# Kernel tuning notes

Hardware: AMD Instinct MI355X
Metric: run time of the kernel (lower is better)

The kernel has to match this reference:

```python
import jax, jax.numpy as jnp
import numpy as np

THRESH = 6.0   # latent_dist_threshold
SCALE = 1.0    # reward_scale
EPS = 1e-6


def _count_scatter(idx, vals):
    # idx, vals: [B, V, N]; counts[b,v,s] = sum of vals over queries whose argmin == s
    B, V, N = idx.shape
    bi = jnp.arange(B)[:, None, None]
    vi = jnp.arange(V)[None, :, None]
    return jnp.zeros((B, V, N), jnp.int32).at[bi, vi, idx].add(vals)


def _direction(min_dists, min_idx, query_xy, source_xy, query_mask):
    # one chamfer direction: queries matched to nearest source particles
    d = jnp.take_along_axis(source_xy, min_idx[..., None], axis=2)  # [B,V,N,2]
    dist = jnp.linalg.norm(query_xy - d, ord=2, axis=-1)            # [B,V,N]
    latent_mask = min_dists > THRESH
    rpm = query_mask | latent_mask                                   # reward_particle_mask
    vals = jnp.where(rpm, 0, 1).astype(jnp.int32)
    count = _count_scatter(min_idx, vals)                            # density counts per source
    w = 1.0 / (jnp.take_along_axis(count, min_idx, axis=2).astype(jnp.float32) + EPS)
    dist = jnp.where(rpm, 0.0, w * dist)
    unmatched = jnp.any((~query_mask) & latent_mask, axis=-1).astype(jnp.float32)
    groups = jnp.maximum(jnp.sum(count > 0, axis=2).astype(jnp.float32) + unmatched, 1.0)
    return -(jnp.sum(dist, axis=2) + unmatched) / groups             # [B,V]


def setup_inputs() -> dict:
    key = jax.random.key(0)
    k1, k2 = jax.random.split(key)
    achieved = jax.random.normal(k1, (256, 2, 512, 10), dtype=jnp.float32)
    desired = jax.random.normal(k2, (256, 2, 512, 10), dtype=jnp.float32)
    return {"achieved": achieved, "desired": desired}


def reference(achieved, desired):
    # latent_classifier=None -> obj_class_cond = ones -> mask = (ones == 0) = all False
    state_mask = jnp.zeros(achieved.shape[:-1], bool)
    goal_mask = jnp.zeros(desired.shape[:-1], bool)
    s_vis = achieved[..., 5:9]
    s_xy = achieved[..., :2]
    g_vis = desired[..., 5:9]
    g_xy = desired[..., :2]
    # 'l2_simple' pairwise squared dist: P[b,v,i,j] = ||s_vis_i - g_vis_j||^2
    P = (jnp.sum(s_vis ** 2, -1)[..., :, None]
         + jnp.sum(g_vis ** 2, -1)[..., None, :]
         - 2.0 * jnp.einsum('bvnd,bvmd->bvnm', s_vis, g_vis))
    P = jnp.where(state_mask[..., :, None] | goal_mask[..., None, :], jnp.inf, P)
    # goal -> state: min over state axis (2)
    md1 = jnp.min(P, axis=2)
    mi1 = jnp.argmin(P, axis=2).astype(jnp.int32)
    r_g2s = _direction(md1, mi1, g_xy, s_xy, goal_mask)
    # state -> goal: min over goal axis (3)
    md2 = jnp.min(P, axis=3)
    mi2 = jnp.argmin(P, axis=3).astype(jnp.int32)
    r_s2g = _direction(md2, mi2, s_xy, g_xy, state_mask)
    rv = (r_g2s + r_s2g) / 2.0                                       # [B,V]
    no_valid = jnp.all(goal_mask, -1) | jnp.all(state_mask, -1)
    rv = jnp.where(no_valid, -1.0, rv)
    reward = jnp.mean(rv, axis=1)
    return SCALE * reward[:, None]                                    # [B,1]
```

## Files before the change

kernel.cpp:

```cpp
#include <hip/hip_runtime.h>
#include <math.h>

#define NB 256
#define NV 2
#define NN 512
#define ND 10
#define THRESH_SQ 6.0f
#define EPS_W 1e-6f

typedef __attribute__((ext_vector_type(8))) short bf16x8;
typedef __attribute__((ext_vector_type(4))) float f32x4;

__device__ __forceinline__ unsigned short f2bf(float x) {
    union { float f; unsigned u; } v; v.f = x;
    unsigned r = v.u + 0x7FFFu + ((v.u >> 16) & 1u);
    return (unsigned short)(r >> 16);
}
__device__ __forceinline__ float bf2f(unsigned short h) {
    union { unsigned u; float f; } v; v.u = ((unsigned)h) << 16; return v.f;
}
__device__ __forceinline__ void split3(float x, unsigned short* s) {
    unsigned short h = f2bf(x); float r = x - bf2f(h);
    unsigned short m = f2bf(r); float r2 = r - bf2f(m);
    s[0] = h; s[1] = m; s[2] = f2bf(r2);
}
__device__ __forceinline__ unsigned umin_(unsigned a, unsigned b) { return a < b ? a : b; }

__device__ __forceinline__ int recaddr(int c, int row) {
    return (c << 13) + ((row << 4) ^ (c << 5));
}

__global__ __launch_bounds__(512, 4)
void chamfer_bv(const float* __restrict__ achieved,
                const float* __restrict__ desired,
                float* __restrict__ rv_out)
{
    const int bv  = blockIdx.x;
    const int tid = threadIdx.x;

    __shared__ __align__(16) char buf[32768];
    __shared__ __align__(16) unsigned colKey[NN * 4];

    const float* arow = achieved + ((size_t)bv * NN + tid) * ND;
    const float* drow = desired  + ((size_t)bv * NN + tid) * ND;

    const unsigned short ONE = 0x3F80;
    const int pi[6] = {0,0,1,2,1,0};
    const int pj[6] = {0,1,0,0,1,2};

    const float g5 = drow[5], g6 = drow[6], g7 = drow[7], g8 = drow[8];

    {
        float a5 = arow[5], a6 = arow[6], a7 = arow[7], a8 = arow[8];
        unsigned short us[4][3];
        split3(-2.0f*a5, us[0]); split3(-2.0f*a6, us[1]);
        split3(-2.0f*a7, us[2]); split3(-2.0f*a8, us[3]);
        float sn2 = a5*a5 + a6*a6 + a7*a7 + a8*a8;
        unsigned short sn[3]; split3(sn2, sn);
        unsigned short t[32];
        #pragma unroll
        for (int d = 0; d < 4; ++d)
            #pragma unroll
            for (int p = 0; p < 6; ++p)
                t[d*6+p] = us[d][pi[p]];
        t[24]=sn[0]; t[25]=sn[1]; t[26]=sn[2];
        t[27]=ONE;   t[28]=ONE;   t[29]=ONE;
        t[30]=ONE;   t[31]=0;
        #pragma unroll
        for (int c = 0; c < 4; ++c) {
            bf16x8 v;
            #pragma unroll
            for (int e = 0; e < 8; ++e) v[e] = (short)t[c*8+e];
            *(bf16x8*)(buf + recaddr(c, tid)) = v;
        }
    }
    #pragma unroll
    for (int c = 0; c < 4; ++c) colKey[tid + c*512] = 0xFFFFFFFFu;
    __syncthreads();

    const int lane = tid & 63, wid = tid >> 6;
    const int lrow = lane & 15, lchk = lane >> 4;

    bf16x8 afr[4];
    #pragma unroll
    for (int nt = 0; nt < 4; ++nt)
        afr[nt] = *(const bf16x8*)(buf + recaddr(lchk, (wid<<6) + (nt<<4) + lrow));
    __syncthreads();

    {
        unsigned short gs[4][3];
        split3(g5, gs[0]); split3(g6, gs[1]); split3(g7, gs[2]); split3(g8, gs[3]);
        float gn2 = g5*g5 + g6*g6 + g7*g7 + g8*g8;
        unsigned short gn[3]; split3(gn2, gn);
        unsigned short t[32];
        #pragma unroll
        for (int d = 0; d < 4; ++d)
            #pragma unroll
            for (int p = 0; p < 6; ++p)
                t[d*6+p] = gs[d][pj[p]];
        t[24]=ONE;   t[25]=ONE;   t[26]=ONE;
        t[27]=gn[0]; t[28]=gn[1]; t[29]=gn[2];
        t[30]=0x3A80; t[31]=0;
        #pragma unroll
        for (int c = 0; c < 4; ++c) {
            bf16x8 v;
            #pragma unroll
            for (int e = 0; e < 8; ++e) v[e] = (short)t[c*8+e];
            *(bf16x8*)(buf + recaddr(c, tid)) = v;
        }
    }
    __syncthreads();

    unsigned rowKey[4][4];
    int ncst[4][4];
    #pragma unroll
    for (int nt = 0; nt < 4; ++nt)
        #pragma unroll
        for (int j = 0; j < 4; ++j) {
            rowKey[nt][j] = 0xFFFFFFFFu;
            ncst[nt][j]   = (wid<<6) + (nt<<4) + (lchk<<2) + j;
        }

    const unsigned MASK = 0xFFFFFE00u;
    const f32x4 z = {0.0f, 0.0f, 0.0f, 0.0f};

    bf16x8 bfr = *(const bf16x8*)(buf + recaddr(lchk, lrow));
    #pragma unroll 4
    for (int mt = 0; mt < 32; ++mt) {
        const int mtn = (mt + 1) & 31;
        bf16x8 bnext = *(const bf16x8*)(buf + recaddr(lchk, (mtn<<4) + lrow));
        const unsigned mcur = (unsigned)((mt<<4) + lrow);
        unsigned cp0, cp1, cp2, cp3;
        #pragma unroll
        for (int nt = 0; nt < 4; ++nt) {
            f32x4 acc = __builtin_amdgcn_mfma_f32_16x16x32_bf16(afr[nt], bfr, z, 0, 0, 0);
            unsigned b0 = __float_as_uint(acc[0]) & MASK;
            unsigned b1 = __float_as_uint(acc[1]) & MASK;
            unsigned b2 = __float_as_uint(acc[2]) & MASK;
            unsigned b3 = __float_as_uint(acc[3]) & MASK;
            rowKey[nt][0] = umin_(rowKey[nt][0], b0 | mcur);
            rowKey[nt][1] = umin_(rowKey[nt][1], b1 | mcur);
            rowKey[nt][2] = umin_(rowKey[nt][2], b2 | mcur);
            rowKey[nt][3] = umin_(rowKey[nt][3], b3 | mcur);
            unsigned k0 = b0 | (unsigned)ncst[nt][0];
            unsigned k1 = b1 | (unsigned)ncst[nt][1];
            unsigned k2 = b2 | (unsigned)ncst[nt][2];
            unsigned k3 = b3 | (unsigned)ncst[nt][3];
            unsigned cp = umin_(umin_(k0, k1), umin_(k2, k3));
            if (nt == 0) cp0 = cp; else if (nt == 1) cp1 = cp;
            else if (nt == 2) cp2 = cp; else cp3 = cp;
        }
        unsigned cv = umin_(umin_(cp0, cp1), umin_(cp2, cp3));
        atomicMin(&colKey[(mcur << 2) | lchk], cv);
        bfr = bnext;
    }

    #pragma unroll
    for (int nt = 0; nt < 4; ++nt) {
        #pragma unroll
        for (int j = 0; j < 4; ++j) {
            unsigned v = rowKey[nt][j];
            #pragma unroll
            for (int s = 1; s <= 8; s <<= 1)
                v = umin_(v, (unsigned)__shfl_xor((int)v, s));
            rowKey[nt][j] = v;
        }
    }
    __syncthreads();

    unsigned* rowKeyArr = (unsigned*)buf;
    int*      cnt       = (int*)(buf + 2048);
    float*    redF      = (float*)(buf + 4096);
    int*      redI      = (int*)(buf + 4160);

    if (lrow == 0) {
        #pragma unroll
        for (int nt = 0; nt < 4; ++nt)
            #pragma unroll
            for (int j = 0; j < 4; ++j)
                rowKeyArr[ncst[nt][j]] = rowKey[nt][j];
    }
    cnt[tid] = 0;
    __syncthreads();

    const uint4 ck = *(const uint4*)&colKey[tid << 2];
    const unsigned kA = umin_(umin_(ck.x, ck.y), umin_(ck.z, ck.w));
    const unsigned kB = rowKeyArr[tid];
    const int miA = (int)(kA & 0x1FFu);
    const int miB = (int)(kB & 0x1FFu);
    const bool latA = __uint_as_float(kA & MASK) > THRESH_SQ;
    const bool latB = __uint_as_float(kB & MASK) > THRESH_SQ;
    if (!latA) atomicAdd(&cnt[miA], 1);
    if (!latB) atomicAdd(&cnt[miB], 0x10000);
    __syncthreads();

    float sumA = 0.0f, sumB = 0.0f;
    if (!latA) {
        const float* sp = achieved + ((size_t)bv * NN + miA) * ND;
        float dx = drow[0] - sp[0], dy = drow[1] - sp[1];
        float w = 1.0f / ((float)(cnt[miA] & 0xFFFF) + EPS_W);
        sumA = w * sqrtf(dx*dx + dy*dy);
    }
    if (!latB) {
        const float* gp = desired + ((size_t)bv * NN + miB) * ND;
        float dx = arow[0] - gp[0], dy = arow[1] - gp[1];
        float w = 1.0f / ((float)(((unsigned)cnt[miB]) >> 16) + EPS_W);
        sumB = w * sqrtf(dx*dx + dy*dy);
    }
    const int c0i = cnt[tid];
    int grpPk = ((c0i & 0xFFFF) ? 1 : 0) | ((((unsigned)c0i) >> 16) ? 0x10000 : 0);
    int latPk = (latA ? 1 : 0) | (latB ? 2 : 0);

    #pragma unroll
    for (int off = 32; off > 0; off >>= 1) {
        sumA  += __shfl_down(sumA, off);
        sumB  += __shfl_down(sumB, off);
        grpPk += __shfl_down(grpPk, off);
        latPk |= __shfl_down(latPk, off);
    }
    if (lane == 0) {
        redF[wid*2] = sumA; redF[wid*2+1] = sumB;
        redI[wid*2] = grpPk; redI[wid*2+1] = latPk;
    }
    __syncthreads();
    if (tid == 0) {
        float sA = 0.0f, sB = 0.0f; int G = 0, L = 0;
        #pragma unroll
        for (int w2 = 0; w2 < 8; ++w2) {
            sA += redF[w2*2]; sB += redF[w2*2+1];
            G  += redI[w2*2]; L |= redI[w2*2+1];
        }
        float unmA = (L & 1) ? 1.0f : 0.0f;
        float unmB = (L & 2) ? 1.0f : 0.0f;
        float gA = (float)(G & 0xFFFF), gB = (float)(((unsigned)G) >> 16);
        float rA = -(sA + unmA) / fmaxf(gA + unmA, 1.0f);
        float rB = -(sB + unmB) / fmaxf(gB + unmB, 1.0f);
        rv_out[bv] = 0.5f * (rA + rB);
    }
}

__global__ void chamfer_finalize(const float* __restrict__ rv, float* __restrict__ out)
{
    int b = blockIdx.x * 256 + threadIdx.x;
    if (b < NB) out[b] = 0.5f * (rv[2*b] + rv[2*b + 1]);
}

extern "C" void kernel_launch(void* const* d_in, const int* in_sizes, int n_in,
                              void* d_out, int out_size, void* d_ws, size_t ws_size,
                              hipStream_t stream)
{
    const float* achieved = (const float*)d_in[0];
    const float* desired  = (const float*)d_in[1];
    float* out = (float*)d_out;
    float* rv  = (float*)d_ws;

    chamfer_bv<<<NB * NV, 512, 0, stream>>>(achieved, desired, rv);
    chamfer_finalize<<<1, 256, 0, stream>>>(rv, out);
}
```

Baseline: 30.21 us.

## Double block to 1024 threads with separate A/B LDS buffers

Launches 1024 threads per (b,v) block instead of 512, so each wave handles 32 state rows (2 MFMA tiles) instead of 64. State and goal records are packed concurrently by the two halves of the block into separate LDS buffers, which removes a sync and the buffer reuse phase. The goal is more waves per block to hide MFMA and LDS latency, but LDS use grows to about 72KB per block and colKey atomics double, which may cut the number of resident blocks.

```diff
diff --git a/kernel.cpp b/kernel.cpp
--- a/kernel.cpp
+++ b/kernel.cpp
@@ -30,7 +30,7 @@
     return (c << 13) + ((row << 4) ^ (c << 5));
 }
 
-__global__ __launch_bounds__(512, 4)
+__global__ __launch_bounds__(1024, 4)
 void chamfer_bv(const float* __restrict__ achieved,
                 const float* __restrict__ desired,
                 float* __restrict__ rv_out)
@@ -38,19 +38,15 @@
     const int bv  = blockIdx.x;
     const int tid = threadIdx.x;
 
-    __shared__ __align__(16) char buf[32768];
+    __shared__ __align__(16) char bufA[32768];
+    __shared__ __align__(16) char bufB[32768];
     __shared__ __align__(16) unsigned colKey[NN * 4];
 
-    const float* arow = achieved + ((size_t)bv * NN + tid) * ND;
-    const float* drow = desired  + ((size_t)bv * NN + tid) * ND;
-
     const unsigned short ONE = 0x3F80;
-    const int pi[6] = {0,0,1,2,1,0};
-    const int pj[6] = {0,1,0,0,1,2};
-
-    const float g5 = drow[5], g6 = drow[6], g7 = drow[7], g8 = drow[8];
-
-    {
+
+    if (tid < NN) {
+        const int pi[6] = {0,0,1,2,1,0};
+        const float* arow = achieved + ((size_t)bv * NN + tid) * ND;
         float a5 = arow[5], a6 = arow[6], a7 = arow[7], a8 = arow[8];
         unsigned short us[4][3];
         split3(-2.0f*a5, us[0]); split3(-2.0f*a6, us[1]);
@@ -71,23 +67,13 @@
             bf16x8 v;
             #pragma unroll
             for (int e = 0; e < 8; ++e) v[e] = (short)t[c*8+e];
-            *(bf16x8*)(buf + recaddr(c, tid)) = v;
-        }
-    }
-    #pragma unroll
-    for (int c = 0; c < 4; ++c) colKey[tid + c*512] = 0xFFFFFFFFu;
-    __syncthreads();
-
-    const int lane = tid & 63, wid = tid >> 6;
-    const int lrow = lane & 15, lchk = lane >> 4;
-
-    bf16x8 afr[4];
-    #pragma unroll
-    for (int nt = 0; nt < 4; ++nt)
-        afr[nt] = *(const bf16x8*)(buf + recaddr(lchk, (wid<<6) + (nt<<4) + lrow));
-    __syncthreads();
-
-    {
+            *(bf16x8*)(bufA + recaddr(c, tid)) = v;
+        }
+    } else {
+        const int pj[6] = {0,1,0,0,1,2};
+        const int r = tid - NN;
+        const float* drow = desired + ((size_t)bv * NN + r) * ND;
+        float g5 = drow[5], g6 = drow[6], g7 = drow[7], g8 = drow[8];
         unsigned short gs[4][3];
         split3(g5, gs[0]); split3(g6, gs[1]); split3(g7, gs[2]); split3(g8, gs[3]);
         float gn2 = g5*g5 + g6*g6 + g7*g7 + g8*g8;
@@ -106,33 +92,43 @@
             bf16x8 v;
             #pragma unroll
             for (int e = 0; e < 8; ++e) v[e] = (short)t[c*8+e];
-            *(bf16x8*)(buf + recaddr(c, tid)) = v;
-        }
-    }
-    __syncthreads();
-
-    unsigned rowKey[4][4];
-    int ncst[4][4];
-    #pragma unroll
-    for (int nt = 0; nt < 4; ++nt)
+            *(bf16x8*)(bufB + recaddr(c, r)) = v;
+        }
+    }
+    colKey[tid]        = 0xFFFFFFFFu;
+    colKey[tid + 1024] = 0xFFFFFFFFu;
+    __syncthreads();
+
+    const int lane = tid & 63, wid = tid >> 6;
+    const int lrow = lane & 15, lchk = lane >> 4;
+
+    bf16x8 afr[2];
+    #pragma unroll
+    for (int nt = 0; nt < 2; ++nt)
+        afr[nt] = *(const bf16x8*)(bufA + recaddr(lchk, (wid<<5) + (nt<<4) + lrow));
+
+    unsigned rowKey[2][4];
+    int ncst[2][4];
+    #pragma unroll
+    for (int nt = 0; nt < 2; ++nt)
         #pragma unroll
         for (int j = 0; j < 4; ++j) {
             rowKey[nt][j] = 0xFFFFFFFFu;
-            ncst[nt][j]   = (wid<<6) + (nt<<4) + (lchk<<2) + j;
+            ncst[nt][j]   = (wid<<5) + (nt<<4) + (lchk<<2) + j;
         }
 
     const unsigned MASK = 0xFFFFFE00u;
     const f32x4 z = {0.0f, 0.0f, 0.0f, 0.0f};
 
-    bf16x8 bfr = *(const bf16x8*)(buf + recaddr(lchk, lrow));
+    bf16x8 bfr = *(const bf16x8*)(bufB + recaddr(lchk, lrow));
     #pragma unroll 4
     for (int mt = 0; mt < 32; ++mt) {
         const int mtn = (mt + 1) & 31;
-        bf16x8 bnext = *(const bf16x8*)(buf + recaddr(lchk, (mtn<<4) + lrow));
+        bf16x8 bnext = *(const bf16x8*)(bufB + recaddr(lchk, (mtn<<4) + lrow));
         const unsigned mcur = (unsigned)((mt<<4) + lrow);
-        unsigned cp0, cp1, cp2, cp3;
-        #pragma unroll
-        for (int nt = 0; nt < 4; ++nt) {
+        unsigned cp0, cp1;
+        #pragma unroll
+        for (int nt = 0; nt < 2; ++nt) {
             f32x4 acc = __builtin_amdgcn_mfma_f32_16x16x32_bf16(afr[nt], bfr, z, 0, 0, 0);
             unsigned b0 = __float_as_uint(acc[0]) & MASK;
             unsigned b1 = __float_as_uint(acc[1]) & MASK;
@@ -147,16 +143,15 @@
             unsigned k2 = b2 | (unsigned)ncst[nt][2];
             unsigned k3 = b3 | (unsigned)ncst[nt][3];
             unsigned cp = umin_(umin_(k0, k1), umin_(k2, k3));
-            if (nt == 0) cp0 = cp; else if (nt == 1) cp1 = cp;
-            else if (nt == 2) cp2 = cp; else cp3 = cp;
-        }
-        unsigned cv = umin_(umin_(cp0, cp1), umin_(cp2, cp3));
+            if (nt == 0) cp0 = cp; else cp1 = cp;
+        }
+        unsigned cv = umin_(cp0, cp1);
         atomicMin(&colKey[(mcur << 2) | lchk], cv);
         bfr = bnext;
     }
 
     #pragma unroll
-    for (int nt = 0; nt < 4; ++nt) {
+    for (int nt = 0; nt < 2; ++nt) {
         #pragma unroll
         for (int j = 0; j < 4; ++j) {
             unsigned v = rowKey[nt][j];
@@ -168,48 +163,57 @@
     }
     __syncthreads();
 
-    unsigned* rowKeyArr = (unsigned*)buf;
-    int*      cnt       = (int*)(buf + 2048);
-    float*    redF      = (float*)(buf + 4096);
-    int*      redI      = (int*)(buf + 4160);
+    unsigned* rowKeyArr = (unsigned*)bufA;
+    int*      cnt       = (int*)(bufA + 2048);
+    float*    redF      = (float*)(bufA + 4096);
+    int*      redI      = (int*)(bufA + 4224);
 
     if (lrow == 0) {
         #pragma unroll
-        for (int nt = 0; nt < 4; ++nt)
+        for (int nt = 0; nt < 2; ++nt)
             #pragma unroll
             for (int j = 0; j < 4; ++j)
                 rowKeyArr[ncst[nt][j]] = rowKey[nt][j];
     }
-    cnt[tid] = 0;
-    __syncthreads();
-
-    const uint4 ck = *(const uint4*)&colKey[tid << 2];
-    const unsigned kA = umin_(umin_(ck.x, ck.y), umin_(ck.z, ck.w));
-    const unsigned kB = rowKeyArr[tid];
-    const int miA = (int)(kA & 0x1FFu);
-    const int miB = (int)(kB & 0x1FFu);
-    const bool latA = __uint_as_float(kA & MASK) > THRESH_SQ;
-    const bool latB = __uint_as_float(kB & MASK) > THRESH_SQ;
-    if (!latA) atomicAdd(&cnt[miA], 1);
-    if (!latB) atomicAdd(&cnt[miB], 0x10000);
+    if (tid < NN) cnt[tid] = 0;
     __syncthreads();
 
     float sumA = 0.0f, sumB = 0.0f;
-    if (!latA) {
-        const float* sp = achieved + ((size_t)bv * NN + miA) * ND;
-        float dx = drow[0] - sp[0], dy = drow[1] - sp[1];
-        float w = 1.0f / ((float)(cnt[miA] & 0xFFFF) + EPS_W);
-        sumA = w * sqrtf(dx*dx + dy*dy);
-    }
-    if (!latB) {
-        const float* gp = desired + ((size_t)bv * NN + miB) * ND;
-        float dx = arow[0] - gp[0], dy = arow[1] - gp[1];
-        float w = 1.0f / ((float)(((unsigned)cnt[miB]) >> 16) + EPS_W);
-        sumB = w * sqrtf(dx*dx + dy*dy);
-    }
-    const int c0i = cnt[tid];
-    int grpPk = ((c0i & 0xFFFF) ? 1 : 0) | ((((unsigned)c0i) >> 16) ? 0x10000 : 0);
-    int latPk = (latA ? 1 : 0) | (latB ? 2 : 0);
+    int grpPk = 0, latPk = 0;
+    int miA = 0, miB = 0;
+    bool latA = false, latB = false;
+    if (tid < NN) {
+        const uint4 ck = *(const uint4*)&colKey[tid << 2];
+        const unsigned kA = umin_(umin_(ck.x, ck.y), umin_(ck.z, ck.w));
+        const unsigned kB = rowKeyArr[tid];
+        miA = (int)(kA & 0x1FFu);
+        miB = (int)(kB & 0x1FFu);
+        latA = __uint_as_float(kA & MASK) > THRESH_SQ;
+        latB = __uint_as_float(kB & MASK) > THRESH_SQ;
+        if (!latA) atomicAdd(&cnt[miA], 1);
+        if (!latB) atomicAdd(&cnt[miB], 0x10000);
+    }
+    __syncthreads();
+
+    if (tid < NN) {
+        const float* arow_e = achieved + ((size_t)bv * NN + tid) * ND;
+        const float* drow_e = desired  + ((size_t)bv * NN + tid) * ND;
+        if (!latA) {
+            const float* sp = achieved + ((size_t)bv * NN + miA) * ND;
+            float dx = drow_e[0] - sp[0], dy = drow_e[1] - sp[1];
+            float w = 1.0f / ((float)(cnt[miA] & 0xFFFF) + EPS_W);
+            sumA = w * sqrtf(dx*dx + dy*dy);
+        }
+        if (!latB) {
+            const float* gp = desired + ((size_t)bv * NN + miB) * ND;
+            float dx = arow_e[0] - gp[0], dy = arow_e[1] - gp[1];
+            float w = 1.0f / ((float)(((unsigned)cnt[miB]) >> 16) + EPS_W);
+            sumB = w * sqrtf(dx*dx + dy*dy);
+        }
+        const int c0i = cnt[tid];
+        grpPk = ((c0i & 0xFFFF) ? 1 : 0) | ((((unsigned)c0i) >> 16) ? 0x10000 : 0);
+        latPk = (latA ? 1 : 0) | (latB ? 2 : 0);
+    }
 
     #pragma unroll
     for (int off = 32; off > 0; off >>= 1) {
@@ -226,7 +230,7 @@
     if (tid == 0) {
         float sA = 0.0f, sB = 0.0f; int G = 0, L = 0;
         #pragma unroll
-        for (int w2 = 0; w2 < 8; ++w2) {
+        for (int w2 = 0; w2 < 16; ++w2) {
             sA += redF[w2*2]; sB += redF[w2*2+1];
             G  += redI[w2*2]; L |= redI[w2*2+1];
         }
@@ -254,6 +258,6 @@
     float* out = (float*)d_out;
     float* rv  = (float*)d_ws;
 
-    chamfer_bv<<<NB * NV, 512, 0, stream>>>(achieved, desired, rv);
+    chamfer_bv<<<NB * NV, 1024, 0, stream>>>(achieved, desired, rv);
     chamfer_finalize<<<1, 256, 0, stream>>>(rv, out);
 }
```

Result: no change. 30.76 us (+1.8%).
